# Kernel tuning notes

Hardware: AMD Instinct MI355X
Metric: run time of the kernel (lower is better)

## Reference

```python
import jax, jax.numpy as jnp
import numpy as np

B, S, H, NH, P = 1, 2048, 1024, 16, 2
D = H // NH
SCALE = 1.0 / np.sqrt(D).astype(np.float32)


def _lin(x, W, b):
    # x: [..., in] @ W: [in, out] + b: [out]
    return x @ W + b


def _split_heads(x):
    # [..., S, H] -> [..., NH, S, D]
    return x.reshape(*x.shape[:-2], x.shape[-2], NH, D).swapaxes(-3, -2)


def _merge_heads(x):
    # [..., NH, S, D] -> [..., S, H]
    return x.swapaxes(-3, -2).reshape(*x.shape[:-3], x.shape[-2], H)


def setup_inputs() -> dict:
    key = jax.random.key(0)
    ks = jax.random.split(key, 20)
    w = lambda k, i, o: jax.random.normal(k, (i, o), jnp.float32) * 0.02
    inp = {
        "hidden_states": jax.random.normal(ks[0], (B, S, H), jnp.float32),
        "past_states": jax.random.normal(ks[1], (P, B, S, H), jnp.float32),
        "Wq": w(ks[2], H, H), "bq": jnp.zeros((H,), jnp.float32),
        "Wk": w(ks[3], H, H), "bk": jnp.zeros((H,), jnp.float32),
        "Wv": w(ks[4], H, H), "bv": jnp.zeros((H,), jnp.float32),
        "Wo": w(ks[5], H, H), "bo": jnp.zeros((H,), jnp.float32),
        "Wrq": w(ks[6], H, H), "brq": jnp.zeros((H,), jnp.float32),
        "Wrk": w(ks[7], H, H), "brk": jnp.zeros((H,), jnp.float32),
        "Wrv": w(ks[8], H, H), "brv": jnp.zeros((H,), jnp.float32),
        "Wg": w(ks[9], 2 * H, H), "bg": jnp.zeros((H,), jnp.float32),
    }
    return inp


def reference(hidden_states, past_states, Wq, bq, Wk, bk, Wv, bv, Wo, bo,
              Wrq, brq, Wrk, brk, Wrv, brv, Wg, bg):
    # --- standard self-attention ---
    q = _split_heads(_lin(hidden_states, Wq, bq))  # [B,NH,S,D]
    k = _split_heads(_lin(hidden_states, Wk, bk))
    v = _split_heads(_lin(hidden_states, Wv, bv))
    scores = jnp.einsum('bhsd,bhtd->bhst', q, k) * SCALE
    attn = jax.nn.softmax(scores, axis=-1)
    ctx = jnp.einsum('bhst,bhtd->bhsd', attn, v)
    output = _lin(_merge_heads(ctx), Wo, bo)  # [B,S,H]

    # --- recursive attention over past states (recursion_level > 0) ---
    rq = _split_heads(_lin(output, Wrq, brq))           # [B,NH,S,D]
    rk = _split_heads(_lin(past_states, Wrk, brk))      # [P,B,NH,S,D]
    rv = _split_heads(_lin(past_states, Wrv, brv))
    rscores = jnp.einsum('bhsd,pbhtd->pbhst', rq, rk) * SCALE
    rattn = jax.nn.softmax(rscores, axis=-1)
    rctx = jnp.einsum('pbhst,pbhtd->pbhsd', rattn, rv)
    recursive_output = _merge_heads(rctx).mean(axis=0)  # [B,S,H]

    gate = jax.nn.sigmoid(_lin(jnp.concatenate([output, recursive_output], axis=-1), Wg, bg))
    output = output * (1.0 - gate) + recursive_output * gate
    return output
```

## Files before the change

### kernel.cpp

```cpp
#include <hip/hip_runtime.h>
#include <hip/hip_bf16.h>

#define S_LEN 2048
#define HDIM  1024
#define NHEAD 16
#define DHEAD 64
#define QSCALE  (0.125f * 1.44269504088896340736f)

typedef __bf16 bf16;
typedef __bf16 bf16x4 __attribute__((ext_vector_type(4)));
typedef __bf16 bf16x8 __attribute__((ext_vector_type(8)));
typedef float  f32x4  __attribute__((ext_vector_type(4)));

#define MFMA16(a,b,c) __builtin_amdgcn_mfma_f32_16x16x32_bf16((a),(b),(c),0,0,0)

__device__ __forceinline__ void gload16(const bf16* g, bf16* lds_wave_base) {
  __builtin_amdgcn_global_load_lds(
      (const __attribute__((address_space(1))) void*)g,
      (__attribute__((address_space(3))) void*)lds_wave_base, 16, 0, 0);
}

__global__ void cvt_f32_bf16_kernel(const float* __restrict__ in,
                                    bf16* __restrict__ out, int n4) {
  int i = blockIdx.x * blockDim.x + threadIdx.x;
  int stride = gridDim.x * blockDim.x;
  for (; i < n4; i += stride) {
    float4 v = ((const float4*)in)[i];
    bf16x4 o = { (bf16)v.x, (bf16)v.y, (bf16)v.z, (bf16)v.w };
    ((bf16x4*)out)[i] = o;
  }
}

struct TrJob { const float* in; bf16* out; };
struct TrArgs { TrJob j[8]; };

__global__ void transp_cvt_kernel(TrArgs args, int rows, int cols) {
  TrJob t = args.j[blockIdx.z];
  __shared__ float tile[32][33];
  int tx = threadIdx.x, ty = threadIdx.y;
  int c0 = blockIdx.x * 32, r0 = blockIdx.y * 32;
  for (int j = ty; j < 32; j += 8)
    tile[j][tx] = t.in[(size_t)(r0 + j) * cols + c0 + tx];
  __syncthreads();
  for (int j = ty; j < 32; j += 8)
    t.out[(size_t)(c0 + j) * rows + r0 + tx] = (bf16)tile[tx][j];
}

struct ThJob { const bf16* in; bf16* out; };
struct ThArgs { ThJob j[4]; };

__global__ void transp_head_kernel(ThArgs args) {
  ThJob t = args.j[blockIdx.z >> 4];
  int h = blockIdx.z & 15;
  __shared__ bf16 tile[32][33];
  int t0 = blockIdx.x * 32, d0 = blockIdx.y * 32;
  int tx = threadIdx.x, ty = threadIdx.y;
  for (int j = ty; j < 32; j += 8)
    tile[j][tx] = t.in[(size_t)(t0 + j) * HDIM + h * DHEAD + d0 + tx];
  __syncthreads();
  for (int j = ty; j < 32; j += 8)
    t.out[((size_t)h * DHEAD + d0 + j) * S_LEN + t0 + tx] = tile[tx][j];
}

struct GemmJob { const bf16* A; const bf16* Bt; const float* bias; bf16* Cb; float* Cf; float cscale; };
struct GemmArgs { GemmJob j[8]; };

__launch_bounds__(256)
__global__ void gemm_bt_kernel(GemmArgs args, int M, int N, int K) {
  GemmJob jb = args.j[blockIdx.z];
  const int bn = blockIdx.x, bm = blockIdx.y;
  const int tid = threadIdx.x;
  const int wave = tid >> 6, lane = tid & 63;
  const int wr = wave >> 1, wc = wave & 1;
  const int l16 = lane & 15, lq = lane >> 4;

  __shared__ alignas(16) bf16 As[2][64 * 32];
  __shared__ alignas(16) bf16 Bs[2][128 * 32];

  f32x4 acc[2][4];
#pragma unroll
  for (int i = 0; i < 2; ++i)
#pragma unroll
    for (int j = 0; j < 4; ++j) acc[i][j] = (f32x4){0.f, 0.f, 0.f, 0.f};

  const bf16* Ap = jb.A + (size_t)bm * 64 * K;
  const bf16* Bp = jb.Bt + (size_t)bn * 128 * K;

  const int c0 = wave * 64 + lane;
  const int r0 = c0 >> 2, c08 = (c0 & 3) << 3;

  auto STAGE = [&](int buf, int kt) {
    gload16(Ap + (size_t)r0 * K + kt + c08, &As[buf][wave * 512]);
    gload16(Bp + (size_t)r0 * K + kt + c08, &Bs[buf][wave * 512]);
    gload16(Bp + (size_t)(r0 + 64) * K + kt + c08, &Bs[buf][2048 + wave * 512]);
  };

  const int NT = K >> 5;
  STAGE(0, 0);
  __syncthreads();

  for (int t = 0; t < NT; ++t) {
    const int cur = t & 1;
    const int ktn = (t + 1 < NT) ? (t + 1) * 32 : t * 32;
    STAGE(cur ^ 1, ktn);

    bf16x8 af[2], bfr[4];
#pragma unroll
    for (int i = 0; i < 2; ++i)
      af[i] = *(const bf16x8*)(&As[cur][(wr * 32 + i * 16 + l16) * 32 + lq * 8]);
#pragma unroll
    for (int j = 0; j < 4; ++j)
      bfr[j] = *(const bf16x8*)(&Bs[cur][(wc * 64 + j * 16 + l16) * 32 + lq * 8]);
#pragma unroll
    for (int i = 0; i < 2; ++i)
#pragma unroll
      for (int j = 0; j < 4; ++j)
        acc[i][j] = MFMA16(af[i], bfr[j], acc[i][j]);

    __syncthreads();
  }

#pragma unroll
  for (int i = 0; i < 2; ++i) {
#pragma unroll
    for (int j = 0; j < 4; ++j) {
      int row0 = bm * 64 + wr * 32 + i * 16 + lq * 4;
      int col  = bn * 128 + wc * 64 + j * 16 + l16;
      float bv = jb.bias ? jb.bias[col] : 0.0f;
#pragma unroll
      for (int r = 0; r < 4; ++r) {
        float v = (acc[i][j][r] + bv) * jb.cscale;
        size_t off = (size_t)(row0 + r) * N + col;
        if (jb.Cb) jb.Cb[off] = (bf16)v;
        if (jb.Cf) jb.Cf[off] = v;
      }
    }
  }
}

__launch_bounds__(256)
__global__ void flash_attn_kernel(const bf16* __restrict__ Q,
                                  const bf16* __restrict__ Kin,
                                  const bf16* __restrict__ VT,
                                  bf16* __restrict__ Ob,
                                  float* __restrict__ Of,
                                  size_t kStride, size_t vStride, size_t oStride) {
  const int qb = blockIdx.x, h = blockIdx.y, p = blockIdx.z;
  const bf16* Kp = Kin + (size_t)p * kStride;
  const bf16* Vp = VT + (size_t)p * vStride;
  const int tid = threadIdx.x;
  const int wave = tid >> 6, lane = tid & 63;
  const int l16 = lane & 15, lq = lane >> 4;

  __shared__ alignas(16) bf16 Ks[2][64][72];
  __shared__ alignas(16) bf16 Vs[2][64][72];
  __shared__ alignas(16) bf16 Ps[4][16][72];

  const int i0 = tid, i1 = tid + 256;
  const int ra = i0 >> 3, ca = (i0 & 7) << 3;
  const int rb = i1 >> 3, cb = (i1 & 7) << 3;

  bf16x8 krg[2], vrg[2];
  auto LOAD_TILE = [&](int tb) {
    krg[0] = *(const bf16x8*)(Kp + (size_t)(tb * 64 + ra) * HDIM + h * DHEAD + ca);
    krg[1] = *(const bf16x8*)(Kp + (size_t)(tb * 64 + rb) * HDIM + h * DHEAD + cb);
    vrg[0] = *(const bf16x8*)(Vp + ((size_t)h * DHEAD + ra) * S_LEN + tb * 64 + ca);
    vrg[1] = *(const bf16x8*)(Vp + ((size_t)h * DHEAD + rb) * S_LEN + tb * 64 + cb);
  };
  auto STORE_TILE = [&](int buf) {
    *(bf16x8*)(&Ks[buf][ra][ca]) = krg[0];
    *(bf16x8*)(&Ks[buf][rb][cb]) = krg[1];
    *(bf16x8*)(&Vs[buf][ra][ca]) = vrg[0];
    *(bf16x8*)(&Vs[buf][rb][cb]) = vrg[1];
  };

  bf16x8 qf[2];
  {
    const bf16* qptr = Q + (size_t)(qb * 64 + wave * 16 + l16) * HDIM + h * DHEAD + lq * 8;
    qf[0] = *(const bf16x8*)qptr;
    qf[1] = *(const bf16x8*)(qptr + 32);
  }

  float m_run = -1e30f, l_run = 0.f;
  f32x4 oacc[4];
#pragma unroll
  for (int j = 0; j < 4; ++j) oacc[j] = (f32x4){0.f, 0.f, 0.f, 0.f};

  const int NT = S_LEN / 64;
  LOAD_TILE(0);
  STORE_TILE(0);
  __syncthreads();

  for (int tb = 0; tb < NT; ++tb) {
    const int cur = tb & 1;
    const bool more = (tb + 1 < NT);
    if (more) LOAD_TILE(tb + 1);

    f32x4 sf[4];
#pragma unroll
    for (int j = 0; j < 4; ++j) sf[j] = (f32x4){0.f, 0.f, 0.f, 0.f};
#pragma unroll
    for (int j = 0; j < 4; ++j)
#pragma unroll
      for (int kk = 0; kk < 2; ++kk) {
        bf16x8 kf = *(const bf16x8*)(&Ks[cur][j * 16 + l16][kk * 32 + lq * 8]);
        sf[j] = MFMA16(kf, qf[kk], sf[j]);
      }

    float mx = -1e30f;
#pragma unroll
    for (int j = 0; j < 4; ++j)
#pragma unroll
      for (int r = 0; r < 4; ++r) mx = fmaxf(mx, sf[j][r]);
    mx = fmaxf(mx, __shfl_xor(mx, 16));
    mx = fmaxf(mx, __shfl_xor(mx, 32));

    float mnew = fmaxf(m_run, mx);
    float corr = exp2f(m_run - mnew);
    m_run = mnew;

    float rs = 0.f;
#pragma unroll
    for (int j = 0; j < 4; ++j)
#pragma unroll
      for (int r = 0; r < 4; ++r) {
        float pv = exp2f(sf[j][r] - mnew);
        sf[j][r] = pv;
        rs += pv;
      }
    rs += __shfl_xor(rs, 16);
    rs += __shfl_xor(rs, 32);
    l_run = l_run * corr + rs;
#pragma unroll
    for (int j = 0; j < 4; ++j) {
      oacc[j][0] *= corr; oacc[j][1] *= corr; oacc[j][2] *= corr; oacc[j][3] *= corr;
    }

#pragma unroll
    for (int j = 0; j < 4; ++j) {
      bf16x4 pk = { (bf16)sf[j][0], (bf16)sf[j][1], (bf16)sf[j][2], (bf16)sf[j][3] };
      *(bf16x4*)(&Ps[wave][l16][j * 16 + lq * 4]) = pk;
    }
    asm volatile("s_waitcnt lgkmcnt(0)" ::: "memory");

    bf16x8 pf[2];
    pf[0] = *(const bf16x8*)(&Ps[wave][l16][lq * 8]);
    pf[1] = *(const bf16x8*)(&Ps[wave][l16][32 + lq * 8]);
#pragma unroll
    for (int j = 0; j < 4; ++j)
#pragma unroll
      for (int kk = 0; kk < 2; ++kk) {
        bf16x8 vtf = *(const bf16x8*)(&Vs[cur][j * 16 + l16][kk * 32 + lq * 8]);
        oacc[j] = MFMA16(vtf, pf[kk], oacc[j]);
      }

    if (more) {
      STORE_TILE(cur ^ 1);
      __syncthreads();
    }
  }

  const float inv = 1.0f / l_run;
  const int q = qb * 64 + wave * 16 + l16;
#pragma unroll
  for (int j = 0; j < 4; ++j) {
    size_t off = (size_t)q * HDIM + h * DHEAD + j * 16 + lq * 4;
    float o0 = oacc[j][0] * inv, o1 = oacc[j][1] * inv,
          o2 = oacc[j][2] * inv, o3 = oacc[j][3] * inv;
    if (Ob) {
      bf16x4 ov = { (bf16)o0, (bf16)o1, (bf16)o2, (bf16)o3 };
      *(bf16x4*)(Ob + off) = ov;
    }
    if (Of) {
      float4 ov = { o0, o1, o2, o3 };
      *(float4*)(Of + (size_t)p * oStride + off) = ov;
    }
  }
}

__global__ void mean_gate_prep_kernel(const float* __restrict__ rc,
                                      const bf16* __restrict__ outb,
                                      float* __restrict__ rof,
                                      bf16* __restrict__ acat,
                                      int n) {
  int i = blockIdx.x * blockDim.x + threadIdx.x;
  int stride = gridDim.x * blockDim.x;
  for (; i < n; i += stride) {
    float ro = 0.5f * (rc[i] + rc[i + n]);
    rof[i] = ro;
    int srow = i >> 10, col = i & 1023;
    size_t base = (size_t)srow * 2048;
    acat[base + col] = outb[i];
    acat[base + 1024 + col] = (bf16)ro;
  }
}

__global__ void final_gate_kernel(const float* __restrict__ outf,
                                  const float* __restrict__ rof,
                                  const float* __restrict__ glog,
                                  float* __restrict__ out, int n) {
  int i = blockIdx.x * blockDim.x + threadIdx.x;
  int stride = gridDim.x * blockDim.x;
  for (; i < n; i += stride) {
    float g = 1.0f / (1.0f + __expf(-glog[i]));
    out[i] = outf[i] * (1.0f - g) + rof[i] * g;
  }
}

extern "C" void kernel_launch(void* const* d_in, const int* in_sizes, int n_in,
                              void* d_out, int out_size, void* d_ws, size_t ws_size,
                              hipStream_t stream) {
  const float* hs   = (const float*)d_in[0];
  const float* past = (const float*)d_in[1];
  const float* Wq = (const float*)d_in[2];   const float* bq = (const float*)d_in[3];
  const float* Wk = (const float*)d_in[4];   const float* bk = (const float*)d_in[5];
  const float* Wv = (const float*)d_in[6];   const float* bv = (const float*)d_in[7];
  const float* Wo = (const float*)d_in[8];   const float* bo = (const float*)d_in[9];
  const float* Wrq = (const float*)d_in[10]; const float* brq = (const float*)d_in[11];
  const float* Wrk = (const float*)d_in[12]; const float* brk = (const float*)d_in[13];
  const float* Wrv = (const float*)d_in[14]; const float* brv = (const float*)d_in[15];
  const float* Wg  = (const float*)d_in[16]; const float* bg  = (const float*)d_in[17];

  char* wp = (char*)d_ws;
  auto alloc = [&](size_t bytes) -> void* {
    void* p = (void*)wp;
    wp += (bytes + 255) & ~(size_t)255;
    return p;
  };
  const size_t NE = (size_t)S_LEN * HDIM;

  bf16* hs_b   = (bf16*)alloc(NE * 2);
  bf16* past_b = (bf16*)alloc(2 * NE * 2);
  bf16* Wqt  = (bf16*)alloc((size_t)HDIM * HDIM * 2);
  bf16* Wkt  = (bf16*)alloc((size_t)HDIM * HDIM * 2);
  bf16* Wvt  = (bf16*)alloc((size_t)HDIM * HDIM * 2);
  bf16* Wot  = (bf16*)alloc((size_t)HDIM * HDIM * 2);
  bf16* Wrqt = (bf16*)alloc((size_t)HDIM * HDIM * 2);
  bf16* Wrkt = (bf16*)alloc((size_t)HDIM * HDIM * 2);
  bf16* Wrvt = (bf16*)alloc((size_t)HDIM * HDIM * 2);
  bf16* Wgt  = (bf16*)alloc((size_t)2 * HDIM * HDIM * 2);
  bf16* q_b   = (bf16*)alloc(NE * 2);
  bf16* k_b   = (bf16*)alloc(NE * 2);
  bf16* v_b   = (bf16*)alloc(NE * 2);
  bf16* vT_b  = (bf16*)alloc(NE * 2);
  bf16* ctx_b = (bf16*)alloc(NE * 2);
  bf16* out_b = (bf16*)alloc(NE * 2);
  float* out_f = (float*)alloc(NE * 4);
  bf16* rq_b  = (bf16*)alloc(NE * 2);
  bf16* rk_b  = (bf16*)alloc(2 * NE * 2);
  bf16* rv_b  = (bf16*)alloc(2 * NE * 2);
  bf16* rvT_b = (bf16*)alloc(2 * NE * 2);
  float* rctx_f = (float*)alloc(2 * NE * 4);
  float* ro_f   = (float*)alloc(NE * 4);
  bf16* acat_b  = (bf16*)alloc(2 * NE * 2);
  float* glog_f = (float*)alloc(NE * 4);

  cvt_f32_bf16_kernel<<<2048, 256, 0, stream>>>(hs, hs_b, (int)(NE / 4));
  cvt_f32_bf16_kernel<<<2048, 256, 0, stream>>>(past, past_b, (int)(2 * NE / 4));

  TrArgs ta{};
  ta.j[0] = {Wq, Wqt};  ta.j[1] = {Wk, Wkt};  ta.j[2] = {Wv, Wvt};
  ta.j[3] = {Wo, Wot};  ta.j[4] = {Wrq, Wrqt}; ta.j[5] = {Wrk, Wrkt};
  ta.j[6] = {Wrv, Wrvt};
  transp_cvt_kernel<<<dim3(32, 32, 7), dim3(32, 8), 0, stream>>>(ta, 1024, 1024);
  TrArgs tg{};
  tg.j[0] = {Wg, Wgt};
  transp_cvt_kernel<<<dim3(32, 64, 1), dim3(32, 8), 0, stream>>>(tg, 2048, 1024);

  GemmArgs g1{};
  g1.j[0] = {hs_b,        Wqt,  bq,  q_b,        nullptr, QSCALE};
  g1.j[1] = {hs_b,        Wkt,  bk,  k_b,        nullptr, 1.0f};
  g1.j[2] = {hs_b,        Wvt,  bv,  v_b,        nullptr, 1.0f};
  g1.j[3] = {past_b,      Wrkt, brk, rk_b,       nullptr, 1.0f};
  g1.j[4] = {past_b + NE, Wrkt, brk, rk_b + NE,  nullptr, 1.0f};
  g1.j[5] = {past_b,      Wrvt, brv, rv_b,       nullptr, 1.0f};
  g1.j[6] = {past_b + NE, Wrvt, brv, rv_b + NE,  nullptr, 1.0f};
  gemm_bt_kernel<<<dim3(8, 32, 7), 256, 0, stream>>>(g1, 2048, 1024, 1024);

  ThArgs th{};
  th.j[0] = {v_b, vT_b};
  th.j[1] = {rv_b, rvT_b};
  th.j[2] = {rv_b + NE, rvT_b + NE};
  transp_head_kernel<<<dim3(64, 2, 48), dim3(32, 8), 0, stream>>>(th);

  flash_attn_kernel<<<dim3(32, 16, 1), 256, 0, stream>>>(
      q_b, k_b, vT_b, ctx_b, nullptr, 0, 0, 0);

  GemmArgs g2{};
  g2.j[0] = {ctx_b, Wot, bo, out_b, out_f, 1.0f};
  gemm_bt_kernel<<<dim3(8, 32, 1), 256, 0, stream>>>(g2, 2048, 1024, 1024);

  GemmArgs g3{};
  g3.j[0] = {out_b, Wrqt, brq, rq_b, nullptr, QSCALE};
  gemm_bt_kernel<<<dim3(8, 32, 1), 256, 0, stream>>>(g3, 2048, 1024, 1024);

  flash_attn_kernel<<<dim3(32, 16, 2), 256, 0, stream>>>(
      rq_b, rk_b, rvT_b, nullptr, rctx_f, NE, NE, NE);

  mean_gate_prep_kernel<<<2048, 256, 0, stream>>>(rctx_f, out_b, ro_f, acat_b, (int)NE);

  GemmArgs g4{};
  g4.j[0] = {acat_b, Wgt, bg, nullptr, glog_f, 1.0f};
  gemm_bt_kernel<<<dim3(8, 32, 1), 256, 0, stream>>>(g4, 2048, 1024, 2048);

  final_gate_kernel<<<2048, 256, 0, stream>>>(out_f, ro_f, glog_f, (float*)d_out, (int)NE);
}
```

Measured before the change: 434.5 us.

## Defer softmax rescaling and process two query tiles per wave in recursive attention

Adds lazy online-softmax rescaling: the running max and accumulator correction are updated only when some row's new max exceeds the old one by a threshold, which skips the exp and multiply work on most tiles. Adds a second flash-attention kernel in which each wave handles 32 query rows, two 16-row sub-tiles sharing each K/V fragment read from LDS. This halves the K/V tile loads per query and doubles MFMA work per LDS read, and is used for the two-state recursive attention. In exchange it uses more registers, may lower occupancy, and launches half as many blocks. Deferring the max risks overflow only if scores grow by more than the threshold without triggering an update.

```diff
diff --git a/kernel.cpp b/kernel.cpp
--- a/kernel.cpp
+++ b/kernel.cpp
@@ -6,6 +6,7 @@
 #define NHEAD 16
 #define DHEAD 64
 #define QSCALE  (0.125f * 1.44269504088896340736f)
+#define DEFER_THR 8.0f
 
 typedef __bf16 bf16;
 typedef __bf16 bf16x4 __attribute__((ext_vector_type(4)));
@@ -215,26 +216,29 @@
     mx = fmaxf(mx, __shfl_xor(mx, 16));
     mx = fmaxf(mx, __shfl_xor(mx, 32));
 
-    float mnew = fmaxf(m_run, mx);
-    float corr = exp2f(m_run - mnew);
-    m_run = mnew;
+    if (!__all(mx <= m_run + DEFER_THR)) {
+      float mnew = fmaxf(m_run, mx);
+      float corr = exp2f(m_run - mnew);
+      m_run = mnew;
+      l_run *= corr;
+#pragma unroll
+      for (int j = 0; j < 4; ++j) {
+        oacc[j][0] *= corr; oacc[j][1] *= corr; oacc[j][2] *= corr; oacc[j][3] *= corr;
+      }
+    }
 
     float rs = 0.f;
 #pragma unroll
     for (int j = 0; j < 4; ++j)
 #pragma unroll
       for (int r = 0; r < 4; ++r) {
-        float pv = exp2f(sf[j][r] - mnew);
+        float pv = exp2f(sf[j][r] - m_run);
         sf[j][r] = pv;
         rs += pv;
       }
     rs += __shfl_xor(rs, 16);
     rs += __shfl_xor(rs, 32);
-    l_run = l_run * corr + rs;
-#pragma unroll
-    for (int j = 0; j < 4; ++j) {
-      oacc[j][0] *= corr; oacc[j][1] *= corr; oacc[j][2] *= corr; oacc[j][3] *= corr;
-    }
+    l_run += rs;
 
 #pragma unroll
     for (int j = 0; j < 4; ++j) {
@@ -274,6 +278,166 @@
     if (Of) {
       float4 ov = { o0, o1, o2, o3 };
       *(float4*)(Of + (size_t)p * oStride + off) = ov;
+    }
+  }
+}
+
+__launch_bounds__(256)
+__global__ void flash_attn2_kernel(const bf16* __restrict__ Q,
+                                   const bf16* __restrict__ Kin,
+                                   const bf16* __restrict__ VT,
+                                   bf16* __restrict__ Ob,
+                                   float* __restrict__ Of,
+                                   size_t kStride, size_t vStride, size_t oStride) {
+  const int qb = blockIdx.x, h = blockIdx.y, p = blockIdx.z;
+  const bf16* Kp = Kin + (size_t)p * kStride;
+  const bf16* Vp = VT + (size_t)p * vStride;
+  const int tid = threadIdx.x;
+  const int wave = tid >> 6, lane = tid & 63;
+  const int l16 = lane & 15, lq = lane >> 4;
+
+  __shared__ alignas(16) bf16 Ks[2][64][72];
+  __shared__ alignas(16) bf16 Vs[2][64][72];
+  __shared__ alignas(16) bf16 Ps[4][2][16][72];
+
+  const int i0 = tid, i1 = tid + 256;
+  const int ra = i0 >> 3, ca = (i0 & 7) << 3;
+  const int rb = i1 >> 3, cb = (i1 & 7) << 3;
+
+  bf16x8 krg[2], vrg[2];
+  auto LOAD_TILE = [&](int tb) {
+    krg[0] = *(const bf16x8*)(Kp + (size_t)(tb * 64 + ra) * HDIM + h * DHEAD + ca);
+    krg[1] = *(const bf16x8*)(Kp + (size_t)(tb * 64 + rb) * HDIM + h * DHEAD + cb);
+    vrg[0] = *(const bf16x8*)(Vp + ((size_t)h * DHEAD + ra) * S_LEN + tb * 64 + ca);
+    vrg[1] = *(const bf16x8*)(Vp + ((size_t)h * DHEAD + rb) * S_LEN + tb * 64 + cb);
+  };
+  auto STORE_TILE = [&](int buf) {
+    *(bf16x8*)(&Ks[buf][ra][ca]) = krg[0];
+    *(bf16x8*)(&Ks[buf][rb][cb]) = krg[1];
+    *(bf16x8*)(&Vs[buf][ra][ca]) = vrg[0];
+    *(bf16x8*)(&Vs[buf][rb][cb]) = vrg[1];
+  };
+
+  bf16x8 qf[2][2];
+#pragma unroll
+  for (int s = 0; s < 2; ++s) {
+    const bf16* qptr = Q + (size_t)(qb * 128 + wave * 32 + s * 16 + l16) * HDIM + h * DHEAD + lq * 8;
+    qf[s][0] = *(const bf16x8*)qptr;
+    qf[s][1] = *(const bf16x8*)(qptr + 32);
+  }
+
+  float m_run[2] = { -1e30f, -1e30f }, l_run[2] = { 0.f, 0.f };
+  f32x4 oacc[2][4];
+#pragma unroll
+  for (int s = 0; s < 2; ++s)
+#pragma unroll
+    for (int j = 0; j < 4; ++j) oacc[s][j] = (f32x4){0.f, 0.f, 0.f, 0.f};
+
+  const int NT = S_LEN / 64;
+  LOAD_TILE(0);
+  STORE_TILE(0);
+  __syncthreads();
+
+  for (int tb = 0; tb < NT; ++tb) {
+    const int cur = tb & 1;
+    const bool more = (tb + 1 < NT);
+    if (more) LOAD_TILE(tb + 1);
+
+    f32x4 sf[2][4];
+#pragma unroll
+    for (int s = 0; s < 2; ++s)
+#pragma unroll
+      for (int j = 0; j < 4; ++j) sf[s][j] = (f32x4){0.f, 0.f, 0.f, 0.f};
+#pragma unroll
+    for (int j = 0; j < 4; ++j)
+#pragma unroll
+      for (int kk = 0; kk < 2; ++kk) {
+        bf16x8 kf = *(const bf16x8*)(&Ks[cur][j * 16 + l16][kk * 32 + lq * 8]);
+        sf[0][j] = MFMA16(kf, qf[0][kk], sf[0][j]);
+        sf[1][j] = MFMA16(kf, qf[1][kk], sf[1][j]);
+      }
+
+#pragma unroll
+    for (int s = 0; s < 2; ++s) {
+      float mx = -1e30f;
+#pragma unroll
+      for (int j = 0; j < 4; ++j)
+#pragma unroll
+        for (int r = 0; r < 4; ++r) mx = fmaxf(mx, sf[s][j][r]);
+      mx = fmaxf(mx, __shfl_xor(mx, 16));
+      mx = fmaxf(mx, __shfl_xor(mx, 32));
+
+      if (!__all(mx <= m_run[s] + DEFER_THR)) {
+        float mnew = fmaxf(m_run[s], mx);
+        float corr = exp2f(m_run[s] - mnew);
+        m_run[s] = mnew;
+        l_run[s] *= corr;
+#pragma unroll
+        for (int j = 0; j < 4; ++j) {
+          oacc[s][j][0] *= corr; oacc[s][j][1] *= corr;
+          oacc[s][j][2] *= corr; oacc[s][j][3] *= corr;
+        }
+      }
+
+      float rs = 0.f;
+#pragma unroll
+      for (int j = 0; j < 4; ++j)
+#pragma unroll
+        for (int r = 0; r < 4; ++r) {
+          float pv = exp2f(sf[s][j][r] - m_run[s]);
+          sf[s][j][r] = pv;
+          rs += pv;
+        }
+      rs += __shfl_xor(rs, 16);
+      rs += __shfl_xor(rs, 32);
+      l_run[s] += rs;
+
+#pragma unroll
+      for (int j = 0; j < 4; ++j) {
+        bf16x4 pk = { (bf16)sf[s][j][0], (bf16)sf[s][j][1], (bf16)sf[s][j][2], (bf16)sf[s][j][3] };
+        *(bf16x4*)(&Ps[wave][s][l16][j * 16 + lq * 4]) = pk;
+      }
+    }
+    asm volatile("s_waitcnt lgkmcnt(0)" ::: "memory");
+
+    bf16x8 pf[2][2];
+#pragma unroll
+    for (int s = 0; s < 2; ++s) {
+      pf[s][0] = *(const bf16x8*)(&Ps[wave][s][l16][lq * 8]);
+      pf[s][1] = *(const bf16x8*)(&Ps[wave][s][l16][32 + lq * 8]);
+    }
+#pragma unroll
+    for (int j = 0; j < 4; ++j)
+#pragma unroll
+      for (int kk = 0; kk < 2; ++kk) {
+        bf16x8 vtf = *(const bf16x8*)(&Vs[cur][j * 16 + l16][kk * 32 + lq * 8]);
+        oacc[0][j] = MFMA16(vtf, pf[0][kk], oacc[0][j]);
+        oacc[1][j] = MFMA16(vtf, pf[1][kk], oacc[1][j]);
+      }
+
+    if (more) {
+      STORE_TILE(cur ^ 1);
+      __syncthreads();
+    }
+  }
+
+#pragma unroll
+  for (int s = 0; s < 2; ++s) {
+    const float inv = 1.0f / l_run[s];
+    const int q = qb * 128 + wave * 32 + s * 16 + l16;
+#pragma unroll
+    for (int j = 0; j < 4; ++j) {
+      size_t off = (size_t)q * HDIM + h * DHEAD + j * 16 + lq * 4;
+      float o0 = oacc[s][j][0] * inv, o1 = oacc[s][j][1] * inv,
+            o2 = oacc[s][j][2] * inv, o3 = oacc[s][j][3] * inv;
+      if (Ob) {
+        bf16x4 ov = { (bf16)o0, (bf16)o1, (bf16)o2, (bf16)o3 };
+        *(bf16x4*)(Ob + off) = ov;
+      }
+      if (Of) {
+        float4 ov = { o0, o1, o2, o3 };
+        *(float4*)(Of + (size_t)p * oStride + off) = ov;
+      }
     }
   }
 }
@@ -394,7 +558,7 @@
   g3.j[0] = {out_b, Wrqt, brq, rq_b, nullptr, QSCALE};
   gemm_bt_kernel<<<dim3(8, 32, 1), 256, 0, stream>>>(g3, 2048, 1024, 1024);
 
-  flash_attn_kernel<<<dim3(32, 16, 2), 256, 0, stream>>>(
+  flash_attn2_kernel<<<dim3(16, 16, 2), 256, 0, stream>>>(
       rq_b, rk_b, rvT_b, nullptr, rctx_f, NE, NE, NE);
 
   mean_gate_prep_kernel<<<2048, 256, 0, stream>>>(rctx_f, out_b, ro_f, acat_b, (int)NE);
```

Result: faster. 416.6 us (-4.1%).
